# Optimization experiments

Hardware: AMD Instinct MI355X
Metric: run time of the kernel (lower is better)

## Reference

```python
import math
import jax, jax.numpy as jnp
import numpy as np

R_MIN, R_MAX, R_BINS = 0.0, 10.0, 64
Z_MIN, Z_MAX, Z_BINS = -2.0, 2.0, 64
DR = (R_MAX - R_MIN) / R_BINS
DZ = (Z_MAX - Z_MIN) / Z_BINS
N = 16777216


def setup_inputs() -> dict:
    key = jax.random.key(0)
    k1, k2 = jax.random.split(key)
    positions = jax.random.normal(k1, (N, 3), dtype=jnp.float32)
    masses = jax.random.uniform(k2, (N,), dtype=jnp.float32)
    return {"positions": positions, "masses": masses}


def _volume():
    redge = R_MIN + jnp.arange(R_BINS + 1, dtype=jnp.float32) * DR
    area = math.pi * (redge[1:] ** 2 - redge[:-1] ** 2)  # [R_BINS]
    return area * DZ


def reference(positions, masses):
    r_cyl = jnp.sqrt(positions[:, 0] ** 2 + positions[:, 1] ** 2)
    i = jnp.floor((r_cyl - R_MIN) / DR).astype(jnp.int32)
    j = jnp.floor((positions[:, 2] - Z_MIN) / DZ).astype(jnp.int32)
    gd = (i >= 0) & (i < R_BINS) & (j >= 0) & (j < Z_BINS)
    flat = jnp.where(gd, i * Z_BINS + j, 0)
    w = jnp.where(gd, masses, 0.0)
    mass_in_bin = jnp.zeros((R_BINS * Z_BINS,), dtype=masses.dtype).at[flat].add(w)
    mass_in_bin = mass_in_bin.reshape(R_BINS, Z_BINS)
    surface_density = mass_in_bin / _volume()[:, None]
    return surface_density
```

## Files before the change

kernel.cpp:

```cpp
#include <hip/hip_runtime.h>
#include <math.h>

#define R_BINS 64
#define Z_BINS 64
#define NBINS (R_BINS * Z_BINS)
#define BLOCK 512
#define WAVES_PER_BLOCK 8
#define GRID 1024
#define NPART GRID

#define RBLOCK 512
#define RGRID (NBINS / 64)

static constexpr float DR     = 10.0f / 64.0f;
static constexpr float DZ     = 4.0f  / 64.0f;
static constexpr float INV_DR = 6.4f;
static constexpr float INV_DZ = 16.0f;

__global__ __launch_bounds__(BLOCK) void hist_kernel(const float4* __restrict__ pos4,
                                                     const float* __restrict__ mass,
                                                     float* __restrict__ partials,
                                                     int nchunks) {
    __shared__ float lbins[NBINS];
    __shared__ float4 stage[WAVES_PER_BLOCK][192];

    const int lane = threadIdx.x & 63;
    const int w    = threadIdx.x >> 6;

    for (int b = threadIdx.x; b < NBINS; b += BLOCK) lbins[b] = 0.0f;
    __syncthreads();

    const int totalWaves = gridDim.x * WAVES_PER_BLOCK;
    float* s = (float*)&stage[w][0];

    for (int c = blockIdx.x * WAVES_PER_BLOCK + w; c < nchunks; c += totalWaves) {
        const float4* pb = pos4 + (size_t)192 * c;
        const float4 f0 = pb[lane];
        const float4 f1 = pb[64 + lane];
        const float4 f2 = pb[128 + lane];

        const float* mb = mass + (size_t)256 * c;
        const float m0 = mb[lane];
        const float m1 = mb[64 + lane];
        const float m2 = mb[128 + lane];
        const float m3 = mb[192 + lane];

        stage[w][lane]       = f0;
        stage[w][64 + lane]  = f1;
        stage[w][128 + lane] = f2;
        __asm__ volatile("s_waitcnt lgkmcnt(0)" ::: "memory");
        __builtin_amdgcn_wave_barrier();

        const float ms[4] = {m0, m1, m2, m3};
#pragma unroll
        for (int k = 0; k < 4; ++k) {
            const int p = 64 * k + lane;
            const float x = s[3 * p];
            const float y = s[3 * p + 1];
            const float z = s[3 * p + 2];
            const float r = sqrtf(x * x + y * y);
            const int i = (int)(r * INV_DR);
            const int j = (int)floorf((z + 2.0f) * INV_DZ);
            if (i < R_BINS && (unsigned)j < (unsigned)Z_BINS) {
                atomicAdd(&lbins[i * Z_BINS + j], ms[k]);
            }
        }
        __asm__ volatile("" ::: "memory");
        __builtin_amdgcn_wave_barrier();
    }

    __syncthreads();
    float4* p4 = (float4*)(partials + (size_t)blockIdx.x * NBINS);
    const float4* l4 = (const float4*)lbins;
    p4[threadIdx.x]         = l4[threadIdx.x];
    p4[BLOCK + threadIdx.x] = l4[BLOCK + threadIdx.x];
}

__global__ void tail_kernel(const float* __restrict__ pos,
                            const float* __restrict__ mass,
                            float* __restrict__ partials,
                            int start, int n) {
    const int t = start + blockIdx.x * blockDim.x + threadIdx.x;
    if (t < n) {
        const float x = pos[3 * t], y = pos[3 * t + 1], z = pos[3 * t + 2];
        const float r = sqrtf(x * x + y * y);
        const int i = (int)(r * INV_DR);
        const int j = (int)floorf((z + 2.0f) * INV_DZ);
        if (i < R_BINS && (unsigned)j < (unsigned)Z_BINS) {
            atomicAdd(&partials[i * Z_BINS + j], mass[t]);
        }
    }
}

__global__ __launch_bounds__(RBLOCK) void reduce_finalize(const float* __restrict__ partials,
                                                          float* __restrict__ out) {
    __shared__ float red[RBLOCK];
    const int t   = threadIdx.x;
    const int bl  = t & 63;
    const int grp = t >> 6;
    const int bin = blockIdx.x * 64 + bl;

    float a0 = 0.0f, a1 = 0.0f, a2 = 0.0f, a3 = 0.0f;
    for (int sb = grp; sb < NPART; sb += 32) {
        a0 += partials[(size_t)(sb)      * NBINS + bin];
        a1 += partials[(size_t)(sb + 8)  * NBINS + bin];
        a2 += partials[(size_t)(sb + 16) * NBINS + bin];
        a3 += partials[(size_t)(sb + 24) * NBINS + bin];
    }
    red[t] = (a0 + a1) + (a2 + a3);
    __syncthreads();

    if (t < 64) {
        float acc = 0.0f;
#pragma unroll
        for (int g = 0; g < 8; ++g) acc += red[g * 64 + bl];
        const int i = bin >> 6;
        const float r0 = (float)i * DR;
        const float r1 = (float)(i + 1) * DR;
        const float area = (float)M_PI * (r1 * r1 - r0 * r0);
        out[bin] = acc / (area * DZ);
    }
}

extern "C" void kernel_launch(void* const* d_in, const int* in_sizes, int n_in,
                              void* d_out, int out_size, void* d_ws, size_t ws_size,
                              hipStream_t stream) {
    const float* positions = (const float*)d_in[0];
    const float* masses    = (const float*)d_in[1];
    float* out      = (float*)d_out;
    float* partials = (float*)d_ws;

    const int n = in_sizes[1];
    const int nchunks = n / 256;
    const int rem = n - nchunks * 256;

    hist_kernel<<<GRID, BLOCK, 0, stream>>>((const float4*)positions, masses,
                                            partials, nchunks);
    if (rem > 0) {
        tail_kernel<<<(rem + 255) / 256, 256, 0, stream>>>(positions, masses,
                                                           partials, nchunks * 256, n);
    }
    reduce_finalize<<<RGRID, RBLOCK, 0, stream>>>(partials, out);
}
```

Before: 335.9 us.

## Load four particles per thread directly via float4, dropping LDS staging

Each thread now reads three float4 position vectors and one float4 of masses, covering four whole particles, and bins them directly. This replaces the per-wave LDS staging that transposed coalesced loads into per-particle order. The aim is to cut LDS traffic and wave barriers. The trade-off is that each load instruction now has a 48-byte per-lane stride, which is less well coalesced across the wavefront.

After: 334.7 us. About the same (-0.4%).

```diff
diff --git a/kernel.cpp b/kernel.cpp
--- a/kernel.cpp
+++ b/kernel.cpp
@@ -5,7 +5,6 @@
 #define Z_BINS 64
 #define NBINS (R_BINS * Z_BINS)
 #define BLOCK 512
-#define WAVES_PER_BLOCK 8
 #define GRID 1024
 #define NPART GRID
 
@@ -17,56 +16,38 @@
 static constexpr float INV_DR = 6.4f;
 static constexpr float INV_DZ = 16.0f;
 
+__device__ __forceinline__ void bin1(float x, float y, float z, float m,
+                                     float* __restrict__ lbins) {
+    const float r = sqrtf(x * x + y * y);
+    const int i = (int)(r * INV_DR);
+    const int j = (int)floorf((z + 2.0f) * INV_DZ);
+    if (i < R_BINS && (unsigned)j < (unsigned)Z_BINS) {
+        atomicAdd(&lbins[i * Z_BINS + j], m);
+    }
+}
+
 __global__ __launch_bounds__(BLOCK) void hist_kernel(const float4* __restrict__ pos4,
-                                                     const float* __restrict__ mass,
+                                                     const float4* __restrict__ mass4,
                                                      float* __restrict__ partials,
-                                                     int nchunks) {
+                                                     int ngroups) {
     __shared__ float lbins[NBINS];
-    __shared__ float4 stage[WAVES_PER_BLOCK][192];
-
-    const int lane = threadIdx.x & 63;
-    const int w    = threadIdx.x >> 6;
 
     for (int b = threadIdx.x; b < NBINS; b += BLOCK) lbins[b] = 0.0f;
     __syncthreads();
 
-    const int totalWaves = gridDim.x * WAVES_PER_BLOCK;
-    float* s = (float*)&stage[w][0];
+    const int total = gridDim.x * BLOCK;
+#pragma unroll 2
+    for (int g = blockIdx.x * BLOCK + threadIdx.x; g < ngroups; g += total) {
+        const size_t gb = (size_t)g * 3;
+        const float4 q0 = pos4[gb];
+        const float4 q1 = pos4[gb + 1];
+        const float4 q2 = pos4[gb + 2];
+        const float4 m  = mass4[g];
 
-    for (int c = blockIdx.x * WAVES_PER_BLOCK + w; c < nchunks; c += totalWaves) {
-        const float4* pb = pos4 + (size_t)192 * c;
-        const float4 f0 = pb[lane];
-        const float4 f1 = pb[64 + lane];
-        const float4 f2 = pb[128 + lane];
-
-        const float* mb = mass + (size_t)256 * c;
-        const float m0 = mb[lane];
-        const float m1 = mb[64 + lane];
-        const float m2 = mb[128 + lane];
-        const float m3 = mb[192 + lane];
-
-        stage[w][lane]       = f0;
-        stage[w][64 + lane]  = f1;
-        stage[w][128 + lane] = f2;
-        __asm__ volatile("s_waitcnt lgkmcnt(0)" ::: "memory");
-        __builtin_amdgcn_wave_barrier();
-
-        const float ms[4] = {m0, m1, m2, m3};
-#pragma unroll
-        for (int k = 0; k < 4; ++k) {
-            const int p = 64 * k + lane;
-            const float x = s[3 * p];
-            const float y = s[3 * p + 1];
-            const float z = s[3 * p + 2];
-            const float r = sqrtf(x * x + y * y);
-            const int i = (int)(r * INV_DR);
-            const int j = (int)floorf((z + 2.0f) * INV_DZ);
-            if (i < R_BINS && (unsigned)j < (unsigned)Z_BINS) {
-                atomicAdd(&lbins[i * Z_BINS + j], ms[k]);
-            }
-        }
-        __asm__ volatile("" ::: "memory");
-        __builtin_amdgcn_wave_barrier();
+        bin1(q0.x, q0.y, q0.z, m.x, lbins);
+        bin1(q0.w, q1.x, q1.y, m.y, lbins);
+        bin1(q1.z, q1.w, q2.x, m.z, lbins);
+        bin1(q2.y, q2.z, q2.w, m.w, lbins);
     }
 
     __syncthreads();
@@ -131,14 +112,15 @@
     float* partials = (float*)d_ws;
 
     const int n = in_sizes[1];
-    const int nchunks = n / 256;
-    const int rem = n - nchunks * 256;
+    const int ngroups = n / 4;
+    const int rem = n - ngroups * 4;
 
-    hist_kernel<<<GRID, BLOCK, 0, stream>>>((const float4*)positions, masses,
-                                            partials, nchunks);
+    hist_kernel<<<GRID, BLOCK, 0, stream>>>((const float4*)positions,
+                                            (const float4*)masses,
+                                            partials, ngroups);
     if (rem > 0) {
         tail_kernel<<<(rem + 255) / 256, 256, 0, stream>>>(positions, masses,
-                                                           partials, nchunks * 256, n);
+                                                           partials, ngroups * 4, n);
     }
     reduce_finalize<<<RGRID, RBLOCK, 0, stream>>>(partials, out);
 }
```
